# Performance work log

Measured on AMD Instinct MI355X. Metric: run time of the kernel, lower is better.

The kernel has to match this reference:

```python
import jax, jax.numpy as jnp
import numpy as np

NUM_EMBEDDINGS = 512
EMBEDDING_DIM = 80
COMMITMENT_COST = 0.25


def setup_inputs() -> dict:
    key = jax.random.key(0)
    kx, kw = jax.random.split(key)
    x = jax.random.normal(kx, (32, EMBEDDING_DIM, 4096), dtype=jnp.float32)  # [B, C, L]
    weight = jax.random.uniform(kw, (NUM_EMBEDDINGS, EMBEDDING_DIM), dtype=jnp.float32)
    return {"x": x, "weight": weight}


def reference(x, weight):
    sg = jax.lax.stop_gradient
    # BCL -> BLC
    inputs = jnp.transpose(x, (0, 2, 1))  # [B, L, C]
    B, L, C = inputs.shape
    flat = inputs.reshape(-1, C)  # [N, C]
    distances = (
        jnp.sum(flat * flat, axis=1, keepdims=True)
        + jnp.sum(weight * weight, axis=1)
        - 2.0 * flat @ weight.T
    )  # [N, K]
    idx = jnp.argmin(distances, axis=1)  # [N]
    # one-hot @ weight == gather
    quantized = weight[idx].reshape(B, L, C)
    e_latent_loss = jnp.mean((sg(quantized) - inputs) ** 2)
    q_latent_loss = jnp.mean((quantized - sg(inputs)) ** 2)
    loss = q_latent_loss + COMMITMENT_COST * e_latent_loss
    # straight-through estimator
    quantized_st = inputs + sg(quantized - inputs)
    # perplexity: avg one-hot probs without materializing encodings
    avg_probs = jnp.bincount(idx, length=NUM_EMBEDDINGS).astype(jnp.float32) / idx.shape[0]
    perplexity = jnp.exp(-jnp.sum(avg_probs * jnp.log(avg_probs + 1e-10)))
    # BLC -> BCL
    return loss, jnp.transpose(quantized_st, (0, 2, 1)), perplexity
```

## Files before the change

### kernel.cpp

```cpp
#include <hip/hip_runtime.h>

#define K_CODES 512
#define DIM 80
#define SEQ 4096
#define NVEC 131072
#define NELEM ((size_t)NVEC * DIM)
#define VPB 128
#define NTILES 32
#define TILE_BYTES 6144

typedef short short8 __attribute__((ext_vector_type(8)));
typedef float f32x4 __attribute__((ext_vector_type(4)));

#define WS_GSQ   2048
#define WS_WSQ   4096
#define WS_WFRAG 8192
#define WS_BK    (8192 + 196608)

__device__ __forceinline__ unsigned short f2bf(float f) {
    union { float f; unsigned int u; } c; c.f = f;
    unsigned int r = c.u + 0x7FFFu + ((c.u >> 16) & 1u);
    return (unsigned short)(r >> 16);
}
__device__ __forceinline__ float bf2f(unsigned short h) {
    union { float f; unsigned int u; } c; c.u = ((unsigned int)h) << 16;
    return c.f;
}

__device__ __forceinline__ void gload_lds16(const void* g, void* l) {
    __builtin_amdgcn_global_load_lds(
        (const __attribute__((address_space(1))) void*)g,
        (__attribute__((address_space(3))) void*)l, 16, 0, 0);
}

__global__ void vq_setup(const float* __restrict__ weight,
                         short8* __restrict__ wf, float* __restrict__ wsq)
{
    int idx = blockIdx.x * 256 + threadIdx.x;
    if (blockIdx.x < 2) {
        int k = blockIdx.x * 256 + threadIdx.x;
        const float* w = weight + (size_t)k * DIM;
        float s = 0.f;
#pragma unroll
        for (int c = 0; c < DIM; ++c) s = fmaf(w[c], w[c], s);
        wsq[k] = s;
    }
    int t   = idx / 384;
    int rem = idx - t * 384;
    int g   = rem >> 6, l = rem & 63;
    int cl  = l & 15, cg = l >> 4;
    int ks  = g % 3, h = g / 3;
    int code = t * 16 + cl;
    int c0 = ks * 32 + cg * 8;
    short8 v;
#pragma unroll
    for (int j = 0; j < 8; ++j) {
        int c = c0 + j;
        unsigned short r = 0;
        if (c < DIM) {
            float f = weight[(size_t)code * DIM + c];
            unsigned short hb = f2bf(f);
            r = h ? f2bf(f - bf2f(hb)) : hb;
        }
        v[j] = (short)r;
    }
    wf[idx] = v;
}

__global__ __launch_bounds__(256, 4) void vq_argmin(
    const float* __restrict__ x, const short8* __restrict__ wf,
    const float* __restrict__ wsq, int* __restrict__ bk)
{
    __shared__ short8 bbuf[2][384];
    __shared__ float wsq_lds[K_CODES];

    const int tid = threadIdx.x;
    *(float2*)&wsq_lds[tid * 2] = *(const float2*)&wsq[tid * 2];

    const int v0 = blockIdx.x * VPB;
    const int b  = v0 >> 12;
    const int l0 = v0 & 4095;
    const float* xbase = x + (size_t)b * DIM * SEQ + l0;

    const int lane = tid & 63, wid = tid >> 6;
    const int cg = lane >> 4;
    const int cl = lane & 15;
    const int ar0 = wid * 32 + cl;
    const int ar1 = ar0 + 16;

    {
        const char* src = (const char*)wf;
        char* dst = (char*)&bbuf[0][0];
        gload_lds16(src + tid * 16, dst + tid * 16);
        if (tid < 128) gload_lds16(src + 4096 + tid * 16, dst + 4096 + tid * 16);
    }

    short8 ahi0[3], alo0[3], ahi1[3], alo1[3];
#pragma unroll
    for (int ks = 0; ks < 3; ++ks) {
#pragma unroll
        for (int j = 0; j < 8; ++j) {
            int c = ks * 32 + cg * 8 + j;
            unsigned short h0 = 0, p0 = 0, h1 = 0, p1 = 0;
            if (c < DIM) {
                float f0 = xbase[(size_t)c * SEQ + ar0];
                float f1 = xbase[(size_t)c * SEQ + ar1];
                h0 = f2bf(f0); p0 = f2bf(f0 - bf2f(h0));
                h1 = f2bf(f1); p1 = f2bf(f1 - bf2f(h1));
            }
            ahi0[ks][j] = (short)h0; alo0[ks][j] = (short)p0;
            ahi1[ks][j] = (short)h1; alo1[ks][j] = (short)p1;
        }
    }

    float bestd[2][4];
    int   bestk[2][4];
#pragma unroll
    for (int s = 0; s < 2; ++s)
#pragma unroll
        for (int r = 0; r < 4; ++r) { bestd[s][r] = 3.4028235e38f; bestk[s][r] = 0; }

    __syncthreads();

    for (int t = 0; t < NTILES; ++t) {
        if (t + 1 < NTILES) {
            const char* src = (const char*)wf + (size_t)(t + 1) * TILE_BYTES;
            char* dst = (char*)&bbuf[(t + 1) & 1][0];
            gload_lds16(src + tid * 16, dst + tid * 16);
            if (tid < 128) gload_lds16(src + 4096 + tid * 16, dst + 4096 + tid * 16);
        }

        const short8* bb = bbuf[t & 1];
        short8 bh0 = bb[lane];
        short8 bh1 = bb[64 + lane];
        short8 bh2 = bb[128 + lane];
        short8 bl0 = bb[192 + lane];
        short8 bl1 = bb[256 + lane];
        short8 bl2 = bb[320 + lane];
        float wv = wsq_lds[t * 16 + cl];

        f32x4 a00 = {0.f,0.f,0.f,0.f}, a01 = {0.f,0.f,0.f,0.f}, a02 = {0.f,0.f,0.f,0.f};
        f32x4 a10 = {0.f,0.f,0.f,0.f}, a11 = {0.f,0.f,0.f,0.f}, a12 = {0.f,0.f,0.f,0.f};
        __builtin_amdgcn_s_setprio(1);
        a00 = __builtin_amdgcn_mfma_f32_16x16x32_bf16(ahi0[0], bh0, a00, 0, 0, 0);
        a01 = __builtin_amdgcn_mfma_f32_16x16x32_bf16(ahi0[1], bh1, a01, 0, 0, 0);
        a02 = __builtin_amdgcn_mfma_f32_16x16x32_bf16(ahi0[2], bh2, a02, 0, 0, 0);
        a10 = __builtin_amdgcn_mfma_f32_16x16x32_bf16(ahi1[0], bh0, a10, 0, 0, 0);
        a11 = __builtin_amdgcn_mfma_f32_16x16x32_bf16(ahi1[1], bh1, a11, 0, 0, 0);
        a12 = __builtin_amdgcn_mfma_f32_16x16x32_bf16(ahi1[2], bh2, a12, 0, 0, 0);
        a00 = __builtin_amdgcn_mfma_f32_16x16x32_bf16(ahi0[0], bl0, a00, 0, 0, 0);
        a01 = __builtin_amdgcn_mfma_f32_16x16x32_bf16(ahi0[1], bl1, a01, 0, 0, 0);
        a02 = __builtin_amdgcn_mfma_f32_16x16x32_bf16(ahi0[2], bl2, a02, 0, 0, 0);
        a10 = __builtin_amdgcn_mfma_f32_16x16x32_bf16(ahi1[0], bl0, a10, 0, 0, 0);
        a11 = __builtin_amdgcn_mfma_f32_16x16x32_bf16(ahi1[1], bl1, a11, 0, 0, 0);
        a12 = __builtin_amdgcn_mfma_f32_16x16x32_bf16(ahi1[2], bl2, a12, 0, 0, 0);
        a00 = __builtin_amdgcn_mfma_f32_16x16x32_bf16(alo0[0], bh0, a00, 0, 0, 0);
        a01 = __builtin_amdgcn_mfma_f32_16x16x32_bf16(alo0[1], bh1, a01, 0, 0, 0);
        a02 = __builtin_amdgcn_mfma_f32_16x16x32_bf16(alo0[2], bh2, a02, 0, 0, 0);
        a10 = __builtin_amdgcn_mfma_f32_16x16x32_bf16(alo1[0], bh0, a10, 0, 0, 0);
        a11 = __builtin_amdgcn_mfma_f32_16x16x32_bf16(alo1[1], bh1, a11, 0, 0, 0);
        a12 = __builtin_amdgcn_mfma_f32_16x16x32_bf16(alo1[2], bh2, a12, 0, 0, 0);
        __builtin_amdgcn_s_setprio(0);

        const int code = t * 16 + cl;
#pragma unroll
        for (int r = 0; r < 4; ++r) {
            float d0 = a00[r] + a01[r] + a02[r];
            float q0 = fmaf(-2.f, d0, wv);
            if (q0 < bestd[0][r]) { bestd[0][r] = q0; bestk[0][r] = code; }
            float d1 = a10[r] + a11[r] + a12[r];
            float q1 = fmaf(-2.f, d1, wv);
            if (q1 < bestd[1][r]) { bestd[1][r] = q1; bestk[1][r] = code; }
        }

        __syncthreads();
    }

#pragma unroll
    for (int s = 0; s < 2; ++s) {
#pragma unroll
        for (int r = 0; r < 4; ++r) {
            float d = bestd[s][r]; int k = bestk[s][r];
#pragma unroll
            for (int off = 1; off < 16; off <<= 1) {
                float od = __shfl_xor(d, off, 64);
                int   ok = __shfl_xor(k, off, 64);
                if (od < d || (od == d && ok < k)) { d = od; k = ok; }
            }
            if (cl == 0) {
                int vloc = wid * 32 + s * 16 + cg * 4 + r;
                bk[v0 + vloc] = k;
            }
        }
    }
}

__global__ __launch_bounds__(256) void vq_epilogue(
    const float* __restrict__ x, const float* __restrict__ weight,
    const int* __restrict__ bk, float* __restrict__ out,
    float* __restrict__ gsq, int* __restrict__ ghist)
{
    __shared__ float lsum[4];
    __shared__ int lhist[K_CODES];
    const int tid = threadIdx.x;
    for (int i = tid; i < K_CODES; i += 256) lhist[i] = 0;
    __syncthreads();

    const int v = blockIdx.x * 256 + tid;
    const int b = v >> 12;
    const int l = v & 4095;
    const int kk = bk[v];
    atomicAdd(&lhist[kk], 1);

    const float* xp = x + (size_t)b * DIM * SEQ + l;
    const float* wr = weight + (size_t)kk * DIM;
    float* op = out + 1 + (size_t)b * DIM * SEQ + l;

    float sq = 0.f;
#pragma unroll
    for (int c = 0; c < DIM; c += 4) {
        float4 wv = *(const float4*)(wr + c);
        float x0 = xp[(size_t)(c + 0) * SEQ];
        float x1 = xp[(size_t)(c + 1) * SEQ];
        float x2 = xp[(size_t)(c + 2) * SEQ];
        float x3 = xp[(size_t)(c + 3) * SEQ];
        float e0 = wv.x - x0, e1 = wv.y - x1, e2 = wv.z - x2, e3 = wv.w - x3;
        sq = fmaf(e0, e0, sq);
        sq = fmaf(e1, e1, sq);
        sq = fmaf(e2, e2, sq);
        sq = fmaf(e3, e3, sq);
        op[(size_t)(c + 0) * SEQ] = wv.x;
        op[(size_t)(c + 1) * SEQ] = wv.y;
        op[(size_t)(c + 2) * SEQ] = wv.z;
        op[(size_t)(c + 3) * SEQ] = wv.w;
    }

#pragma unroll
    for (int off = 32; off; off >>= 1) sq += __shfl_down(sq, off, 64);
    if ((tid & 63) == 0) lsum[tid >> 6] = sq;
    __syncthreads();
    if (tid == 0) {
        float s = lsum[0] + lsum[1] + lsum[2] + lsum[3];
        atomicAdd(gsq, s);
    }
    for (int i = tid; i < K_CODES; i += 256) {
        int cnt = lhist[i];
        if (cnt) atomicAdd(&ghist[i], cnt);
    }
}

__global__ void vq_finalize(const int* __restrict__ hist,
                            const float* __restrict__ gsq,
                            float* __restrict__ out, int out_last)
{
    __shared__ float part[8];
    int t = threadIdx.x;
    float p = (float)hist[t] * (1.0f / (float)NVEC);
    float term = p * logf(p + 1e-10f);
#pragma unroll
    for (int off = 32; off; off >>= 1) term += __shfl_down(term, off, 64);
    if ((t & 63) == 0) part[t >> 6] = term;
    __syncthreads();
    if (t == 0) {
        float s = 0.f;
#pragma unroll
        for (int i = 0; i < 8; ++i) s += part[i];
        out[out_last] = expf(-s);
        out[0] = 1.25f * gsq[0] / (float)NELEM;
    }
}

extern "C" void kernel_launch(void* const* d_in, const int* in_sizes, int n_in,
                              void* d_out, int out_size, void* d_ws, size_t ws_size,
                              hipStream_t stream) {
    const float* x = (const float*)d_in[0];
    const float* weight = (const float*)d_in[1];
    float* out = (float*)d_out;

    int* ghist = (int*)d_ws;
    float* gsq = (float*)((char*)d_ws + WS_GSQ);
    float* wsq = (float*)((char*)d_ws + WS_WSQ);
    short8* wf = (short8*)((char*)d_ws + WS_WFRAG);
    int* bk = (int*)((char*)d_ws + WS_BK);

    hipMemsetAsync(d_ws, 0, 2052, stream);

    vq_setup<<<48, 256, 0, stream>>>(weight, wf, wsq);
    vq_argmin<<<NVEC / VPB, 256, 0, stream>>>(x, wf, wsq, bk);
    vq_epilogue<<<NVEC / 256, 256, 0, stream>>>(x, weight, bk, out, gsq, ghist);
    vq_finalize<<<1, K_CODES, 0, stream>>>(ghist, gsq, out, out_size - 1);
}
```

Baseline: 86.84 us.

## Fuse epilogue into argmin kernel, reusing register-held x splits

The separate epilogue kernel is folded into the argmin kernel. Each lane redistributes its best code indices with a shuffle and writes the quantized output directly. It rebuilds x from the bf16 hi/lo splits already in registers to compute the squared error, and builds the histogram in LDS. This removes the index buffer round trip, a second full read of x, and one kernel launch. Blocks shrink to 128 threads and 64 vectors, which doubles the grid. Reconstructing x from two bf16 halves slightly changes the loss accuracy.

```diff
diff --git a/kernel.cpp b/kernel.cpp
--- a/kernel.cpp
+++ b/kernel.cpp
@@ -5,7 +5,7 @@
 #define SEQ 4096
 #define NVEC 131072
 #define NELEM ((size_t)NVEC * DIM)
-#define VPB 128
+#define VPB 64
 #define NTILES 32
 #define TILE_BYTES 6144
 
@@ -15,7 +15,6 @@
 #define WS_GSQ   2048
 #define WS_WSQ   4096
 #define WS_WFRAG 8192
-#define WS_BK    (8192 + 196608)
 
 __device__ __forceinline__ unsigned short f2bf(float f) {
     union { float f; unsigned int u; } c; c.f = f;
@@ -67,15 +66,19 @@
     wf[idx] = v;
 }
 
-__global__ __launch_bounds__(256, 4) void vq_argmin(
+__global__ __launch_bounds__(128, 4) void vq_argmin(
     const float* __restrict__ x, const short8* __restrict__ wf,
-    const float* __restrict__ wsq, int* __restrict__ bk)
+    const float* __restrict__ wsq, const float* __restrict__ weight,
+    float* __restrict__ out, float* __restrict__ gsq, int* __restrict__ ghist)
 {
     __shared__ short8 bbuf[2][384];
     __shared__ float wsq_lds[K_CODES];
+    __shared__ int lhist[K_CODES];
+    __shared__ float lsum[2];
 
     const int tid = threadIdx.x;
-    *(float2*)&wsq_lds[tid * 2] = *(const float2*)&wsq[tid * 2];
+    *(float4*)&wsq_lds[tid * 4] = *(const float4*)&wsq[tid * 4];
+    for (int i = tid; i < K_CODES; i += 128) lhist[i] = 0;
 
     const int v0 = blockIdx.x * VPB;
     const int b  = v0 >> 12;
@@ -89,10 +92,11 @@
     const int ar1 = ar0 + 16;
 
     {
-        const char* src = (const char*)wf;
-        char* dst = (char*)&bbuf[0][0];
-        gload_lds16(src + tid * 16, dst + tid * 16);
-        if (tid < 128) gload_lds16(src + 4096 + tid * 16, dst + 4096 + tid * 16);
+        const char* src = (const char*)wf + tid * 16;
+        char* dst = (char*)&bbuf[0][0] + tid * 16;
+        gload_lds16(src, dst);
+        gload_lds16(src + 2048, dst + 2048);
+        gload_lds16(src + 4096, dst + 4096);
     }
 
     short8 ahi0[3], alo0[3], ahi1[3], alo1[3];
@@ -124,10 +128,11 @@
 
     for (int t = 0; t < NTILES; ++t) {
         if (t + 1 < NTILES) {
-            const char* src = (const char*)wf + (size_t)(t + 1) * TILE_BYTES;
-            char* dst = (char*)&bbuf[(t + 1) & 1][0];
-            gload_lds16(src + tid * 16, dst + tid * 16);
-            if (tid < 128) gload_lds16(src + 4096 + tid * 16, dst + 4096 + tid * 16);
+            const char* src = (const char*)wf + (size_t)(t + 1) * TILE_BYTES + tid * 16;
+            char* dst = (char*)&bbuf[(t + 1) & 1][0] + tid * 16;
+            gload_lds16(src, dst);
+            gload_lds16(src + 2048, dst + 2048);
+            gload_lds16(src + 4096, dst + 4096);
         }
 
         const short8* bb = bbuf[t & 1];
@@ -187,63 +192,56 @@
                 int   ok = __shfl_xor(k, off, 64);
                 if (od < d || (od == d && ok < k)) { d = od; k = ok; }
             }
-            if (cl == 0) {
-                int vloc = wid * 32 + s * 16 + cg * 4 + r;
-                bk[v0 + vloc] = k;
+            bestk[s][r] = k;
+        }
+    }
+
+    float sq = 0.f;
+    const int r3 = cl & 3;
+    const int srcl = ((cl >> 2) << 4) | r3;
+#pragma unroll
+    for (int s = 0; s < 2; ++s) {
+        int kr = bestk[s][0];
+        kr = (r3 == 1) ? bestk[s][1] : kr;
+        kr = (r3 == 2) ? bestk[s][2] : kr;
+        kr = (r3 == 3) ? bestk[s][3] : kr;
+        const int kv = __shfl(kr, srcl, 64);
+        if (cg == 0) atomicAdd(&lhist[kv], 1);
+
+        const float* wr = weight + (size_t)kv * DIM;
+        const int av = wid * 32 + s * 16 + cl;
+        float* op = out + 1 + (size_t)b * DIM * SEQ + l0 + av;
+
+#pragma unroll
+        for (int ks = 0; ks < 3; ++ks) {
+            const int c0 = ks * 32 + cg * 8;
+            if (c0 < DIM) {
+                float4 wa = *(const float4*)(wr + c0);
+                float4 wb = *(const float4*)(wr + c0 + 4);
+                float w0 = wa.x, w1 = wa.y, w2 = wa.z, w3 = wa.w;
+                float w4 = wb.x, w5 = wb.y, w6 = wb.z, w7 = wb.w;
+#define EMIT(J, WJ)                                                              \
+                {                                                                \
+                    unsigned short hb = (unsigned short)(s ? ahi1[ks][J] : ahi0[ks][J]); \
+                    unsigned short pb = (unsigned short)(s ? alo1[ks][J] : alo0[ks][J]); \
+                    float xr = bf2f(hb) + bf2f(pb);                              \
+                    float e = WJ - xr;                                           \
+                    sq = fmaf(e, e, sq);                                         \
+                    op[(size_t)(c0 + J) * SEQ] = WJ;                             \
+                }
+                EMIT(0, w0) EMIT(1, w1) EMIT(2, w2) EMIT(3, w3)
+                EMIT(4, w4) EMIT(5, w5) EMIT(6, w6) EMIT(7, w7)
+#undef EMIT
             }
         }
     }
-}
-
-__global__ __launch_bounds__(256) void vq_epilogue(
-    const float* __restrict__ x, const float* __restrict__ weight,
-    const int* __restrict__ bk, float* __restrict__ out,
-    float* __restrict__ gsq, int* __restrict__ ghist)
-{
-    __shared__ float lsum[4];
-    __shared__ int lhist[K_CODES];
-    const int tid = threadIdx.x;
-    for (int i = tid; i < K_CODES; i += 256) lhist[i] = 0;
+
+#pragma unroll
+    for (int off = 32; off; off >>= 1) sq += __shfl_down(sq, off, 64);
+    if (lane == 0) lsum[wid] = sq;
     __syncthreads();
-
-    const int v = blockIdx.x * 256 + tid;
-    const int b = v >> 12;
-    const int l = v & 4095;
-    const int kk = bk[v];
-    atomicAdd(&lhist[kk], 1);
-
-    const float* xp = x + (size_t)b * DIM * SEQ + l;
-    const float* wr = weight + (size_t)kk * DIM;
-    float* op = out + 1 + (size_t)b * DIM * SEQ + l;
-
-    float sq = 0.f;
-#pragma unroll
-    for (int c = 0; c < DIM; c += 4) {
-        float4 wv = *(const float4*)(wr + c);
-        float x0 = xp[(size_t)(c + 0) * SEQ];
-        float x1 = xp[(size_t)(c + 1) * SEQ];
-        float x2 = xp[(size_t)(c + 2) * SEQ];
-        float x3 = xp[(size_t)(c + 3) * SEQ];
-        float e0 = wv.x - x0, e1 = wv.y - x1, e2 = wv.z - x2, e3 = wv.w - x3;
-        sq = fmaf(e0, e0, sq);
-        sq = fmaf(e1, e1, sq);
-        sq = fmaf(e2, e2, sq);
-        sq = fmaf(e3, e3, sq);
-        op[(size_t)(c + 0) * SEQ] = wv.x;
-        op[(size_t)(c + 1) * SEQ] = wv.y;
-        op[(size_t)(c + 2) * SEQ] = wv.z;
-        op[(size_t)(c + 3) * SEQ] = wv.w;
-    }
-
-#pragma unroll
-    for (int off = 32; off; off >>= 1) sq += __shfl_down(sq, off, 64);
-    if ((tid & 63) == 0) lsum[tid >> 6] = sq;
-    __syncthreads();
-    if (tid == 0) {
-        float s = lsum[0] + lsum[1] + lsum[2] + lsum[3];
-        atomicAdd(gsq, s);
-    }
-    for (int i = tid; i < K_CODES; i += 256) {
+    if (tid == 0) atomicAdd(gsq, lsum[0] + lsum[1]);
+    for (int i = tid; i < K_CODES; i += 128) {
         int cnt = lhist[i];
         if (cnt) atomicAdd(&ghist[i], cnt);
     }
@@ -281,12 +279,10 @@
     float* gsq = (float*)((char*)d_ws + WS_GSQ);
     float* wsq = (float*)((char*)d_ws + WS_WSQ);
     short8* wf = (short8*)((char*)d_ws + WS_WFRAG);
-    int* bk = (int*)((char*)d_ws + WS_BK);
 
     hipMemsetAsync(d_ws, 0, 2052, stream);
 
     vq_setup<<<48, 256, 0, stream>>>(weight, wf, wsq);
-    vq_argmin<<<NVEC / VPB, 256, 0, stream>>>(x, wf, wsq, bk);
-    vq_epilogue<<<NVEC / 256, 256, 0, stream>>>(x, weight, bk, out, gsq, ghist);
+    vq_argmin<<<NVEC / VPB, 128, 0, stream>>>(x, wf, wsq, weight, out, gsq, ghist);
     vq_finalize<<<1, K_CODES, 0, stream>>>(ghist, gsq, out, out_size - 1);
 }
```

Measured after the change: 126.0 us. 45.1% more time.

## Compute loss from argmin distances instead of rereading x in epilogue

Applied to the files above, without the earlier changes.

The squared error sum is now built inside the argmin kernel as the minimum distance plus the squared norm of x, which is accumulated while x is already being loaded. The epilogue no longer reads x at all and only gathers codebook rows and writes the output. This cuts a full read of x (about 42 MB) from the epilogue. The loss now comes from the expanded distance computed with bf16-split matmuls, which can differ slightly in precision from the direct difference.

```diff
diff --git a/kernel.cpp b/kernel.cpp
--- a/kernel.cpp
+++ b/kernel.cpp
@@ -69,10 +69,12 @@
 
 __global__ __launch_bounds__(256, 4) void vq_argmin(
     const float* __restrict__ x, const short8* __restrict__ wf,
-    const float* __restrict__ wsq, int* __restrict__ bk)
+    const float* __restrict__ wsq, int* __restrict__ bk,
+    float* __restrict__ gsq)
 {
     __shared__ short8 bbuf[2][384];
     __shared__ float wsq_lds[K_CODES];
+    __shared__ float lsum[4];
 
     const int tid = threadIdx.x;
     *(float2*)&wsq_lds[tid * 2] = *(const float2*)&wsq[tid * 2];
@@ -96,6 +98,7 @@
     }
 
     short8 ahi0[3], alo0[3], ahi1[3], alo1[3];
+    float xsq0 = 0.f, xsq1 = 0.f;
 #pragma unroll
     for (int ks = 0; ks < 3; ++ks) {
 #pragma unroll
@@ -105,6 +108,8 @@
             if (c < DIM) {
                 float f0 = xbase[(size_t)c * SEQ + ar0];
                 float f1 = xbase[(size_t)c * SEQ + ar1];
+                xsq0 = fmaf(f0, f0, xsq0);
+                xsq1 = fmaf(f1, f1, xsq1);
                 h0 = f2bf(f0); p0 = f2bf(f0 - bf2f(h0));
                 h1 = f2bf(f1); p1 = f2bf(f1 - bf2f(h1));
             }
@@ -187,20 +192,36 @@
                 int   ok = __shfl_xor(k, off, 64);
                 if (od < d || (od == d && ok < k)) { d = od; k = ok; }
             }
+            bestd[s][r] = d;
+            bestk[s][r] = k;
             if (cl == 0) {
                 int vloc = wid * 32 + s * 16 + cg * 4 + r;
                 bk[v0 + vloc] = k;
             }
         }
     }
+
+    xsq0 += __shfl_xor(xsq0, 16, 64); xsq0 += __shfl_xor(xsq0, 32, 64);
+    xsq1 += __shfl_xor(xsq1, 16, 64); xsq1 += __shfl_xor(xsq1, 32, 64);
+    float sq = 0.f;
+#pragma unroll
+    for (int s = 0; s < 2; ++s) {
+#pragma unroll
+        for (int r = 0; r < 4; ++r) {
+            if (cl == cg * 4 + r) sq += bestd[s][r] + (s ? xsq1 : xsq0);
+        }
+    }
+#pragma unroll
+    for (int off = 32; off; off >>= 1) sq += __shfl_down(sq, off, 64);
+    if (lane == 0) lsum[wid] = sq;
+    __syncthreads();
+    if (tid == 0) atomicAdd(gsq, lsum[0] + lsum[1] + lsum[2] + lsum[3]);
 }
 
 __global__ __launch_bounds__(256) void vq_epilogue(
-    const float* __restrict__ x, const float* __restrict__ weight,
-    const int* __restrict__ bk, float* __restrict__ out,
-    float* __restrict__ gsq, int* __restrict__ ghist)
-{
-    __shared__ float lsum[4];
+    const float* __restrict__ weight, const int* __restrict__ bk,
+    float* __restrict__ out, int* __restrict__ ghist)
+{
     __shared__ int lhist[K_CODES];
     const int tid = threadIdx.x;
     for (int i = tid; i < K_CODES; i += 256) lhist[i] = 0;
@@ -212,37 +233,19 @@
     const int kk = bk[v];
     atomicAdd(&lhist[kk], 1);
 
-    const float* xp = x + (size_t)b * DIM * SEQ + l;
     const float* wr = weight + (size_t)kk * DIM;
     float* op = out + 1 + (size_t)b * DIM * SEQ + l;
 
-    float sq = 0.f;
 #pragma unroll
     for (int c = 0; c < DIM; c += 4) {
         float4 wv = *(const float4*)(wr + c);
-        float x0 = xp[(size_t)(c + 0) * SEQ];
-        float x1 = xp[(size_t)(c + 1) * SEQ];
-        float x2 = xp[(size_t)(c + 2) * SEQ];
-        float x3 = xp[(size_t)(c + 3) * SEQ];
-        float e0 = wv.x - x0, e1 = wv.y - x1, e2 = wv.z - x2, e3 = wv.w - x3;
-        sq = fmaf(e0, e0, sq);
-        sq = fmaf(e1, e1, sq);
-        sq = fmaf(e2, e2, sq);
-        sq = fmaf(e3, e3, sq);
         op[(size_t)(c + 0) * SEQ] = wv.x;
         op[(size_t)(c + 1) * SEQ] = wv.y;
         op[(size_t)(c + 2) * SEQ] = wv.z;
         op[(size_t)(c + 3) * SEQ] = wv.w;
     }
 
-#pragma unroll
-    for (int off = 32; off; off >>= 1) sq += __shfl_down(sq, off, 64);
-    if ((tid & 63) == 0) lsum[tid >> 6] = sq;
-    __syncthreads();
-    if (tid == 0) {
-        float s = lsum[0] + lsum[1] + lsum[2] + lsum[3];
-        atomicAdd(gsq, s);
-    }
+    __syncthreads();
     for (int i = tid; i < K_CODES; i += 256) {
         int cnt = lhist[i];
         if (cnt) atomicAdd(&ghist[i], cnt);
@@ -286,7 +289,7 @@
     hipMemsetAsync(d_ws, 0, 2052, stream);
 
     vq_setup<<<48, 256, 0, stream>>>(weight, wf, wsq);
-    vq_argmin<<<NVEC / VPB, 256, 0, stream>>>(x, wf, wsq, bk);
-    vq_epilogue<<<NVEC / 256, 256, 0, stream>>>(x, weight, bk, out, gsq, ghist);
+    vq_argmin<<<NVEC / VPB, 256, 0, stream>>>(x, wf, wsq, bk, gsq);
+    vq_epilogue<<<NVEC / 256, 256, 0, stream>>>(weight, bk, out, ghist);
     vq_finalize<<<1, K_CODES, 0, stream>>>(ghist, gsq, out, out_size - 1);
 }
```

Measured after the change: 91.35 us. +5.2%, slower.
